# Kernel optimization log

Hardware: AMD Instinct MI355X
Metric: run time of the kernel (lower is better)

Reference implementation:

```python
import jax, jax.numpy as jnp
import numpy as np

B, T, LBL = 256, 1024, 128  # batch, seq_len, label_size (incl. start/end)
NUM = LBL - 2               # real emission labels


def setup_inputs() -> dict:
    key = jax.random.key(0)
    k1, k2, k3, k4 = jax.random.split(key, 4)
    logits = jax.random.normal(k1, (B, T, NUM), jnp.float32)
    labels = jax.random.randint(k2, (B, T), 0, NUM)
    lens = jax.random.randint(k3, (B,), 1, T + 1)  # 1..T inclusive
    transition = jax.random.normal(k4, (LBL, LBL), jnp.float32)
    # CRF.initialize(): nothing may transition INTO start-row source or OUT of end
    transition = transition.at[:, LBL - 1].set(-100.0)
    transition = transition.at[LBL - 2, :].set(-100.0)
    return {"logits": logits, "labels": labels, "lens": lens, "transition": transition}


def reference(logits, labels, lens, transition):
    """CRF negative-free log-likelihood pieces: returns gold_score - norm_score per sequence ([B])."""
    Bb, Tt, num = logits.shape
    L = transition.shape[0]
    start, end = L - 2, L - 1

    # pad_logits: append two -1000 columns for start/end labels -> [B, T, L]
    pads = jnp.full((Bb, Tt, 2), -1000.0, logits.dtype)
    lg = jnp.concatenate([logits, pads], axis=2)

    # ---- gold unary score ----
    mask_t = jnp.arange(Tt)[None, :] < lens[:, None]            # [B, T]
    unary = jnp.take_along_axis(lg, labels[..., None], axis=2)[..., 0]
    unary = jnp.where(mask_t, unary, 0.0).sum(axis=1)

    # ---- gold binary (transition) score ----
    ext = jnp.concatenate(
        [jnp.full((Bb, 1), start, labels.dtype), labels,
         jnp.full((Bb, 1), end, labels.dtype)], axis=1)          # [B, T+2]
    mask_e = jnp.arange(Tt + 2)[None, :] < (lens + 1)[:, None]
    ext = jnp.where(mask_e, ext, end)                            # positions >= len+1 -> end
    trn_scr = transition[ext[:, 1:], ext[:, :-1]]                # [B, T+1] (row=next, col=prev)
    mask_b = jnp.arange(Tt + 1)[None, :] < (lens + 1)[:, None]
    binary = jnp.where(mask_b, trn_scr, 0.0).sum(axis=1)

    gold = unary + binary

    # ---- partition (norm) score via log-sum-exp scan over time ----
    alpha0 = jnp.full((Bb, L), -100.0, lg.dtype).at[:, start].set(0.0)
    lg_t = jnp.transpose(lg, (1, 0, 2))                          # [T, B, L]

    def step(alpha, xs):
        logit, t = xs                                            # logit: [B, L]
        # mat[b, j, i] = logit[b, j] + alpha[b, i] + transition[j, i]
        mat = logit[:, :, None] + alpha[:, None, :] + transition[None]
        alpha_nxt = jax.nn.logsumexp(mat, axis=2)                # [B, L]
        alpha = jnp.where((t < lens)[:, None], alpha_nxt, alpha)
        return alpha, None

    alpha, _ = jax.lax.scan(step, alpha0, (lg_t, jnp.arange(Tt)))
    alpha = alpha + transition[end][None, :]
    norm = jax.nn.logsumexp(alpha, axis=1)                       # [B]

    return gold - norm
```

## Files before the change

kernel.cpp:

```cpp
#include <hip/hip_runtime.h>


typedef _Float16 half_t;
typedef _Float16 h2 __attribute__((ext_vector_type(2)));
typedef _Float16 h8 __attribute__((ext_vector_type(8)));

#define TB  1024
#define NUM 126
#define LBL 128

__device__ __forceinline__ float dot2(h2 a, h2 b, float c) {
  return __builtin_amdgcn_fdot2(a, b, c, false);
}

template <int U>
__device__ __forceinline__ float dotu(h8 a, h8 e, float c) {
  return dot2(__builtin_shufflevector(a, a, 2 * U, 2 * U + 1),
              __builtin_shufflevector(e, e, 2 * U, 2 * U + 1), c);
}

template <int CTRL>
__device__ __forceinline__ float dpp_max_step(float x) {
  int xi = __float_as_int(x);
  int yi = __builtin_amdgcn_update_dpp(xi, xi, CTRL, 0xF, 0xF, false);
  return fmaxf(x, __int_as_float(yi));
}

__device__ __forceinline__ float wave_max64(float x) {
  x = dpp_max_step<0x111>(x);
  x = dpp_max_step<0x112>(x);
  x = dpp_max_step<0x114>(x);
  x = dpp_max_step<0x118>(x);
  x = dpp_max_step<0x142>(x);
  x = dpp_max_step<0x143>(x);
  return __int_as_float(__builtin_amdgcn_readlane(__float_as_int(x), 63));
}

#define LGKM_WAIT() __builtin_amdgcn_s_waitcnt(0xC07F)

__global__ __launch_bounds__(64, 1)
void crf_fwd(const float* __restrict__ logits, const int* __restrict__ labels,
             const int* __restrict__ lens, const float* __restrict__ trans,
             float* __restrict__ out)
{
  const int b  = blockIdx.x;
  const int l  = threadIdx.x;
  const int j0 = l;
  const int j1 = l + 64;
  const int off1 = (j1 < NUM) ? j1 : (NUM - 1);
  const float mask1 = (j1 < NUM) ? 1.0f : 0.0f;
  const int len = lens[b];

  __shared__ h2 a_sh[64];
  h8* a_sh8 = (h8*)a_sh;

  const float* lgbase = logits + (size_t)b * TB * NUM;
  const int*   lab    = labels + (size_t)b * TB;

  h8 E0[16], E1[16];
  {
    const float* tr0 = trans + j0 * LBL;
    const float* tr1 = trans + j1 * LBL;
    #pragma unroll
    for (int q = 0; q < 16; ++q) {
      h8 v0, v1;
      #pragma unroll
      for (int e = 0; e < 8; ++e) {
        int p = 8 * q + e;
        int i = (p >> 1) + 64 * (p & 1);
        v0[e] = (half_t)__expf(tr0[i]);
        v1[e] = (half_t)__expf(tr1[i]);
      }
      E0[q] = v0; E1[q] = v1;
    }
  }

  float g = 0.f;
  #pragma unroll
  for (int kk = 0; kk < 16; ++kk) {
    int t = l + 64 * kk;
    if (t < len) {
      int lt = lab[t];
      int lp = (t == 0) ? (LBL - 2) : lab[t - 1];
      g += lgbase[(size_t)t * NUM + lt] + trans[lt * LBL + lp];
    }
  }
  if (l == 0) g += trans[(LBL - 1) * LBL + lab[len - 1]];
  #pragma unroll
  for (int o = 1; o < 64; o <<= 1) g += __shfl_xor(g, o);
  const float gold = g;

  {
    h2 a_init;
    a_init[0] = (half_t)0.0f;
    a_init[1] = (half_t)((j1 == LBL - 2) ? 1.0f : 0.0f);
    a_sh[l] = a_init;
    LGKM_WAIT();
  }

  float plg0[4], plg1[4];
  #pragma unroll
  for (int d = 0; d < 4; ++d) {
    plg0[d] = lgbase[(size_t)d * NUM + j0];
    plg1[d] = lgbase[(size_t)d * NUM + off1];
  }

  int   Kint = 0;
  int   klast = 0;
  float w0_out = 1.f, w1_out = 1.f;

#define STEP_BODY(Q0, Q1)                                                   \
  {                                                                         \
    float eL0 = __expf(Q0);                                                 \
    float eL1 = __expf(Q1) * mask1;                                         \
    float s0a = 0.f, s0b = 0.f, s1a = 0.f, s1b = 0.f;                       \
    _Pragma("unroll")                                                       \
    for (int q = 0; q < 16; q += 2) {                                       \
      h8 avA = a_sh8[q], avB = a_sh8[q + 1];    \
      h8 e0A = E0[q], e0B = E0[q + 1], e1A = E1[q], e1B = E1[q + 1];        \
      s0a = dotu<0>(avA, e0A, s0a);  s0b = dotu<0>(avB, e0B, s0b);          \
      s1a = dotu<0>(avA, e1A, s1a);  s1b = dotu<0>(avB, e1B, s1b);          \
      s0a = dotu<1>(avA, e0A, s0a);  s0b = dotu<1>(avB, e0B, s0b);          \
      s1a = dotu<1>(avA, e1A, s1a);  s1b = dotu<1>(avB, e1B, s1b);          \
      s0a = dotu<2>(avA, e0A, s0a);  s0b = dotu<2>(avB, e0B, s0b);          \
      s1a = dotu<2>(avA, e1A, s1a);  s1b = dotu<2>(avB, e1B, s1b);          \
      s0a = dotu<3>(avA, e0A, s0a);  s0b = dotu<3>(avB, e0B, s0b);          \
      s1a = dotu<3>(avA, e1A, s1a);  s1b = dotu<3>(avB, e1B, s1b);          \
    }                                                                       \
    float w0 = (s0a + s0b) * eL0;                                           \
    float w1 = (s1a + s1b) * eL1;                                           \
    float m  = wave_max64(fmaxf(w0, w1));               \
    int   k  = (__float_as_int(m) >> 23) - 127;             \
    float sc = __int_as_float((127 - k) << 23);             \
    h2 pk;                                                                  \
    pk[0] = (half_t)(w0 * sc);                                              \
    pk[1] = (half_t)(w1 * sc);                                              \
    a_sh[l] = pk;                                                           \
    LGKM_WAIT();                    \
    Kint += k;                                         \
    klast = k; w0_out = w0; w1_out = w1;                                    \
  }

  int t = 0;
  for (; t + 8 <= len; t += 4) {
    const float* pnext = lgbase + (size_t)(t + 4) * NUM;
    STEP_BODY(plg0[0], plg1[0])
    plg0[0] = pnext[0 * NUM + j0];  plg1[0] = pnext[0 * NUM + off1];
    STEP_BODY(plg0[1], plg1[1])
    plg0[1] = pnext[1 * NUM + j0];  plg1[1] = pnext[1 * NUM + off1];
    STEP_BODY(plg0[2], plg1[2])
    plg0[2] = pnext[2 * NUM + j0];  plg1[2] = pnext[2 * NUM + off1];
    STEP_BODY(plg0[3], plg1[3])
    plg0[3] = pnext[3 * NUM + j0];  plg1[3] = pnext[3 * NUM + off1];
  }
  const int rem = len - t;
  if (rem > 0) STEP_BODY(plg0[0], plg1[0])
  if (rem > 1) STEP_BODY(plg0[1], plg1[1])
  if (rem > 2) STEP_BODY(plg0[2], plg1[2])
  if (rem > 3) STEP_BODY(plg0[3], plg1[3])
  for (int td = t + 4; td < len; ++td) {
    float q0 = lgbase[(size_t)td * NUM + j0];
    float q1 = lgbase[(size_t)td * NUM + off1];
    STEP_BODY(q0, q1)
  }
#undef STEP_BODY

  const float LN2 = 0.6931471805599453f;
  float SigmaPrev = (float)(Kint - klast) * LN2;
  float alpha0 = SigmaPrev + __logf(w0_out);
  float alpha1 = SigmaPrev + __logf(w1_out);

  float v0 = alpha0 + trans[(LBL - 1) * LBL + j0];
  float v1 = alpha1 + trans[(LBL - 1) * LBL + j1];
  float M = wave_max64(fmaxf(v0, v1));
  float p = __expf(v0 - M) + __expf(v1 - M);
  #pragma unroll
  for (int o = 1; o < 64; o <<= 1) p += __shfl_xor(p, o);
  if (l == 0) out[b] = gold - (M + __logf(p));
}

extern "C" void kernel_launch(void* const* d_in, const int* in_sizes, int n_in,
                              void* d_out, int out_size, void* d_ws, size_t ws_size,
                              hipStream_t stream) {
  const float* logits = (const float*)d_in[0];
  const int*   labels = (const int*)d_in[1];
  const int*   lens   = (const int*)d_in[2];
  const float* trans  = (const float*)d_in[3];
  float* out = (float*)d_out;
  (void)in_sizes; (void)n_in; (void)out_size; (void)d_ws; (void)ws_size;
  crf_fwd<<<256, 64, 0, stream>>>(logits, labels, lens, trans, out);
}
```

Baseline: 602.3 us.

## Decouple per-step rescale from wave max using lagged exponent prediction

Each time step now rescales the new alpha by a scale exponent computed from the previous step's wave max, so the DPP max reduction is no longer on the critical path before the LDS store. The explicit LDS waitcnt after each store is removed. The main loop is restructured to run to len-4 with clamped prefetch rows, and the scalar tail loop is dropped. The cost is weaker numerical control: fp16 alpha values could drift toward overflow or underflow when the lag misjudges the scale, and dropping the waitcnt relies on the compiler to order the LDS store before the next read.

New measurement: 581.6 us. -3.4%, faster.

```diff
diff --git a/kernel.cpp b/kernel.cpp
--- a/kernel.cpp
+++ b/kernel.cpp
@@ -35,8 +35,6 @@
   x = dpp_max_step<0x143>(x);
   return __int_as_float(__builtin_amdgcn_readlane(__float_as_int(x), 63));
 }
-
-#define LGKM_WAIT() __builtin_amdgcn_s_waitcnt(0xC07F)
 
 __global__ __launch_bounds__(64, 1)
 void crf_fwd(const float* __restrict__ logits, const int* __restrict__ labels,
@@ -95,7 +93,6 @@
     a_init[0] = (half_t)0.0f;
     a_init[1] = (half_t)((j1 == LBL - 2) ? 1.0f : 0.0f);
     a_sh[l] = a_init;
-    LGKM_WAIT();
   }
 
   float plg0[4], plg1[4];
@@ -105,8 +102,9 @@
     plg1[d] = lgbase[(size_t)d * NUM + off1];
   }
 
-  int   Kint = 0;
-  int   klast = 0;
+  int   P    = 6;
+  int   Kacc = 0;
+  int   Kout = 0;
   float w0_out = 1.f, w1_out = 1.f;
 
 #define STEP_BODY(Q0, Q1)                                                   \
@@ -129,44 +127,45 @@
     }                                                                       \
     float w0 = (s0a + s0b) * eL0;                                           \
     float w1 = (s1a + s1b) * eL1;                                           \
-    float m  = wave_max64(fmaxf(w0, w1));               \
-    int   k  = (__float_as_int(m) >> 23) - 127;             \
-    float sc = __int_as_float((127 - k) << 23);             \
+    float sc = __int_as_float((127 - P) << 23);      \
     h2 pk;                                                                  \
     pk[0] = (half_t)(w0 * sc);                                              \
     pk[1] = (half_t)(w1 * sc);                                              \
-    a_sh[l] = pk;                                                           \
-    LGKM_WAIT();                    \
-    Kint += k;                                         \
-    klast = k; w0_out = w0; w1_out = w1;                                    \
+    a_sh[l] = pk;                        \
+    Kout = Kacc;  Kacc += P;                           \
+    \
+    float m  = wave_max64(fmaxf(w0, w1));                                   \
+    int   Em = ((__float_as_int(m) >> 23) & 0xFF) - 127;                    \
+    P = Em - P + 6;                   \
+    w0_out = w0; w1_out = w1;                                               \
   }
 
   int t = 0;
-  for (; t + 8 <= len; t += 4) {
-    const float* pnext = lgbase + (size_t)(t + 4) * NUM;
+  for (; t + 4 <= len; t += 4) {
+    int r0 = t + 4, r1 = t + 5, r2 = t + 6, r3 = t + 7;
+    r0 = (r0 < TB) ? r0 : (TB - 1);  r1 = (r1 < TB) ? r1 : (TB - 1);
+    r2 = (r2 < TB) ? r2 : (TB - 1);  r3 = (r3 < TB) ? r3 : (TB - 1);
     STEP_BODY(plg0[0], plg1[0])
-    plg0[0] = pnext[0 * NUM + j0];  plg1[0] = pnext[0 * NUM + off1];
+    plg0[0] = lgbase[(size_t)r0 * NUM + j0];
+    plg1[0] = lgbase[(size_t)r0 * NUM + off1];
     STEP_BODY(plg0[1], plg1[1])
-    plg0[1] = pnext[1 * NUM + j0];  plg1[1] = pnext[1 * NUM + off1];
+    plg0[1] = lgbase[(size_t)r1 * NUM + j0];
+    plg1[1] = lgbase[(size_t)r1 * NUM + off1];
     STEP_BODY(plg0[2], plg1[2])
-    plg0[2] = pnext[2 * NUM + j0];  plg1[2] = pnext[2 * NUM + off1];
+    plg0[2] = lgbase[(size_t)r2 * NUM + j0];
+    plg1[2] = lgbase[(size_t)r2 * NUM + off1];
     STEP_BODY(plg0[3], plg1[3])
-    plg0[3] = pnext[3 * NUM + j0];  plg1[3] = pnext[3 * NUM + off1];
+    plg0[3] = lgbase[(size_t)r3 * NUM + j0];
+    plg1[3] = lgbase[(size_t)r3 * NUM + off1];
   }
   const int rem = len - t;
   if (rem > 0) STEP_BODY(plg0[0], plg1[0])
   if (rem > 1) STEP_BODY(plg0[1], plg1[1])
   if (rem > 2) STEP_BODY(plg0[2], plg1[2])
-  if (rem > 3) STEP_BODY(plg0[3], plg1[3])
-  for (int td = t + 4; td < len; ++td) {
-    float q0 = lgbase[(size_t)td * NUM + j0];
-    float q1 = lgbase[(size_t)td * NUM + off1];
-    STEP_BODY(q0, q1)
-  }
 #undef STEP_BODY
 
   const float LN2 = 0.6931471805599453f;
-  float SigmaPrev = (float)(Kint - klast) * LN2;
+  float SigmaPrev = (float)Kout * LN2;
   float alpha0 = SigmaPrev + __logf(w0_out);
   float alpha1 = SigmaPrev + __logf(w1_out);
 
```
